# Performance work log

Measured on AMD Instinct MI355X. Metric: run time of the kernel, lower is better.

The kernel has to match this reference:

```python
import jax, jax.numpy as jnp
import numpy as np

B, C, H, W = 64, 64, 32, 32
K = 1024  # codebook_num
EPS = 1e-10


def setup_inputs() -> dict:
    key = jax.random.key(0)
    kz, kc = jax.random.split(key)
    z = jax.random.normal(kz, (B, C, H, W), dtype=jnp.float32)
    # nn.init.uniform_(codebook.weight, -1/K, 1/K)
    codebook = jax.random.uniform(kc, (K, C), dtype=jnp.float32, minval=-1.0 / K, maxval=1.0 / K)
    return {"z": z, "codebook": codebook}


def reference(z, codebook):
    Bz, Cz, Hz, Wz = z.shape
    flat_z = jnp.transpose(z, (0, 2, 3, 1)).reshape(-1, Cz)  # [N, C]
    dists = (jnp.sum(flat_z ** 2, axis=1, keepdims=True)
             + jnp.sum(codebook ** 2, axis=1)
             - 2.0 * flat_z @ codebook.T)
    indices = jnp.argmin(dists, axis=1)  # [N] int
    quantized_z = codebook[indices].reshape(Bz, Hz, Wz, Cz).transpose(0, 3, 1, 2)
    quantized_z_st = z + jax.lax.stop_gradient(quantized_z - z)
    # perplexity: probs = mean one-hot = histogram / N
    n = indices.shape[0]
    counts = jax.ops.segment_sum(jnp.ones((n,), dtype=jnp.float32), indices, num_segments=K)
    probs = counts / n
    perplexity = jnp.exp(-jnp.sum(probs * jnp.log(jnp.clip(probs, EPS))))
    return quantized_z, quantized_z_st, indices, perplexity
```

## Files before the change

### kernel.cpp

```cpp
#include <hip/hip_runtime.h>
#include <math.h>

#define NVEC   65536
#define CDIM   64
#define KBOOK  1024
#define NTOT   4194304


typedef __bf16 bf16x8 __attribute__((ext_vector_type(8)));
typedef float  f32x4  __attribute__((ext_vector_type(4)));

__global__ void prep_kernel(const float* __restrict__ cb, float* __restrict__ se,
                            int* __restrict__ hist, __bf16* __restrict__ cbT) {
    const int t = blockIdx.x * 256 + threadIdx.x;
    hist[t] = 0;
    const float* row = cb + t * CDIM;
    float r[8];
#pragma unroll
    for (int j = 0; j < 8; ++j) r[j] = __fmul_rn(row[j], row[j]);
#pragma unroll
    for (int i = 8; i < 64; i += 8)
#pragma unroll
        for (int j = 0; j < 8; ++j) r[j] = __fadd_rn(r[j], __fmul_rn(row[i + j], row[i + j]));
    se[t] = __fadd_rn(__fadd_rn(__fadd_rn(r[0], r[1]), __fadd_rn(r[2], r[3])),
                      __fadd_rn(__fadd_rn(r[4], r[5]), __fadd_rn(r[6], r[7])));
    const int tt = t >> 4, la = t & 15;
    __bf16* tb = cbT + (size_t)tt * 2048;
#pragma unroll
    for (int g = 0; g < 4; ++g)
#pragma unroll
        for (int j = 0; j < 8; ++j) {
            const float e0 = row[8 * g + j];
            const float e1 = row[32 + 8 * g + j];
            const __bf16 h0 = (__bf16)e0, h1 = (__bf16)e1;
            const int lo8 = (g * 16 + la) * 8 + j;
            tb[lo8]              = h0;
            tb[512 + lo8]        = h1;
            tb[1024 + lo8]       = (__bf16)(e0 - (float)h0);
            tb[1536 + lo8]       = (__bf16)(e1 - (float)h1);
        }
}

__launch_bounds__(256)
__attribute__((amdgpu_waves_per_eu(4, 4)))
__global__ void approx_kernel(const float* __restrict__ z, const __bf16* __restrict__ cbT,
                              const float* __restrict__ se,
                              unsigned int* __restrict__ cand) {
    const int tid = threadIdx.x;
    const int w = tid >> 6;
    const int l = tid & 63;
    const int la = l & 15;
    const int g  = l >> 4;
    const int n = blockIdx.x * 64 + w * 16 + la;
    const int b = n >> 10, hw = n & 1023;
    const float* zb = z + (size_t)b * (CDIM * 1024) + hw;

    bf16x8 mh0, ml0, mh1, ml1;
#pragma unroll
    for (int j = 0; j < 8; ++j) {
        {
            float zc = zb[(g * 8 + j) * 1024];
            float m  = -2.0f * zc;
            __bf16 h = (__bf16)m;
            mh0[j] = h; ml0[j] = (__bf16)(m - (float)h);
        }
        {
            float zc = zb[(32 + g * 8 + j) * 1024];
            float m  = -2.0f * zc;
            __bf16 h = (__bf16)m;
            mh1[j] = h; ml1[j] = (__bf16)(m - (float)h);
        }
    }

    float b1 = 3.4e38f, b2 = 3.4e38f;
    int   k1 = 0,       k2 = 0;
    const int kv = g * 4;
    const __bf16* tbase = cbT + (size_t)l * 8;

#define DECL_SLOT(s) bf16x8 ah0_##s, ah1_##s, al0_##s, al1_##s; f32x4 se_##s;
    DECL_SLOT(a) DECL_SLOT(b) DECL_SLOT(c) DECL_SLOT(d)
#undef DECL_SLOT

#define LOADT(s, ttv) { const int t_ = (ttv) & 63;                       \
        const __bf16* p_ = tbase + (size_t)t_ * 2048;                    \
        ah0_##s = *(const bf16x8*)(p_);                                  \
        ah1_##s = *(const bf16x8*)(p_ + 512);                            \
        al0_##s = *(const bf16x8*)(p_ + 1024);                           \
        al1_##s = *(const bf16x8*)(p_ + 1536);                           \
        se_##s  = *(const f32x4*)(se + t_ * 16 + kv); }

#define INS1(d_, kt_) { const bool c1 = (d_) < b1, c2 = (d_) < b2;       \
        b2 = c1 ? b1 : (c2 ? (d_) : b2);  k2 = c1 ? k1 : (c2 ? (kt_) : k2); \
        b1 = c1 ? (d_) : b1;              k1 = c1 ? (kt_) : k1; }

#define COMPT(s, ttv) { const int k0_ = (ttv) * 16;                      \
        f32x4 aA = se_##s; f32x4 aB = {0.f, 0.f, 0.f, 0.f};              \
        aA = __builtin_amdgcn_mfma_f32_16x16x32_bf16(ah0_##s, mh0, aA, 0, 0, 0); \
        aB = __builtin_amdgcn_mfma_f32_16x16x32_bf16(ah1_##s, mh1, aB, 0, 0, 0); \
        aA = __builtin_amdgcn_mfma_f32_16x16x32_bf16(al0_##s, mh0, aA, 0, 0, 0); \
        aB = __builtin_amdgcn_mfma_f32_16x16x32_bf16(al1_##s, mh1, aB, 0, 0, 0); \
        aA = __builtin_amdgcn_mfma_f32_16x16x32_bf16(ah0_##s, ml0, aA, 0, 0, 0); \
        aB = __builtin_amdgcn_mfma_f32_16x16x32_bf16(ah1_##s, ml1, aB, 0, 0, 0); \
        { const float d0_ = aA[0] + aB[0]; INS1(d0_, k0_ + kv)     }     \
        { const float d1_ = aA[1] + aB[1]; INS1(d1_, k0_ + kv + 1) }     \
        { const float d2_ = aA[2] + aB[2]; INS1(d2_, k0_ + kv + 2) }     \
        { const float d3_ = aA[3] + aB[3]; INS1(d3_, k0_ + kv + 3) } }

    LOADT(a, 0) LOADT(b, 1)
    for (int tt = 0; tt < 64; tt += 4) {
        LOADT(c, tt + 2) LOADT(d, tt + 3)
        COMPT(a, tt)     COMPT(b, tt + 1)
        LOADT(a, tt + 4) LOADT(b, tt + 5)
        COMPT(c, tt + 2) COMPT(d, tt + 3)
    }
#undef LOADT
#undef INS1
#undef COMPT

    cand[n * 4 + g] = (unsigned int)k1 | ((unsigned int)k2 << 16);
}

__global__ void rescore_kernel(const float* __restrict__ z, const float* __restrict__ cb,
                               const float* __restrict__ se,
                               const unsigned int* __restrict__ cand,
                               unsigned long long* __restrict__ keys,
                               int* __restrict__ hist, float* __restrict__ outIdxF) {
    __shared__ int lh[KBOOK];
    for (int i = threadIdx.x; i < KBOOK; i += 256) lh[i] = 0;
    __syncthreads();

    const int n = blockIdx.x * 256 + threadIdx.x;
    int ks[8];
#pragma unroll
    for (int g = 0; g < 4; ++g) {
        const unsigned int p = cand[n * 4 + g];
        ks[2 * g]     = (int)(p & 0xFFFFu);
        ks[2 * g + 1] = (int)(p >> 16);
    }
    const int b = n >> 10, hw = n & 1023;
    const float* zb = z + (size_t)b * (CDIM * 1024) + hw;

    float zx[64], r[8];
#pragma unroll
    for (int j = 0; j < 8; ++j) {
        const float zc = zb[j * 1024];
        zx[j] = zc + zc;
        r[j] = __fmul_rn(zc, zc);
    }
#pragma unroll
    for (int c = 8; c < 64; ++c) {
        const float zc = zb[c * 1024];
        zx[c] = zc + zc;
        r[c & 7] = __fadd_rn(r[c & 7], __fmul_rn(zc, zc));
    }
    const float sx = __fadd_rn(__fadd_rn(__fadd_rn(r[0], r[1]), __fadd_rn(r[2], r[3])),
                               __fadd_rn(__fadd_rn(r[4], r[5]), __fadd_rn(r[6], r[7])));

    float a[8];
#pragma unroll
    for (int i = 0; i < 8; ++i) a[i] = 0.0f;
    const float4* cb4 = (const float4*)cb;
#pragma unroll
    for (int q = 0; q < 16; ++q) {
#pragma unroll
        for (int i = 0; i < 8; ++i) {
            const float4 ev = cb4[ks[i] * 16 + q];
            a[i] = fmaf(zx[4 * q],     ev.x, a[i]);
            a[i] = fmaf(zx[4 * q + 1], ev.y, a[i]);
            a[i] = fmaf(zx[4 * q + 2], ev.z, a[i]);
            a[i] = fmaf(zx[4 * q + 3], ev.w, a[i]);
        }
    }
    unsigned long long best = ~0ull;
#pragma unroll
    for (int i = 0; i < 8; ++i) {
        const float d = __fsub_rn(__fadd_rn(sx, se[ks[i]]), a[i]);
        unsigned int ob = __float_as_uint(d);
        ob = (ob & 0x80000000u) ? ~ob : (ob | 0x80000000u);
        const unsigned long long key = ((unsigned long long)ob << 32) | (unsigned int)ks[i];
        if (key < best) best = key;
    }
    keys[n] = best;
    const int kbest = (int)(best & 0xFFFFFFFFu);
    outIdxF[n] = (float)kbest;
    atomicAdd(&lh[kbest], 1);
    __syncthreads();
    for (int i = threadIdx.x; i < KBOOK; i += 256)
        if (lh[i]) atomicAdd(&hist[i], lh[i]);
}

__global__ void scatter_kernel(const float* __restrict__ z, const float* __restrict__ cb,
                               const unsigned long long* __restrict__ keys,
                               const int* __restrict__ hist,
                               float* __restrict__ out) {
    const int o = (blockIdx.x * 256 + threadIdx.x) * 4;
    const int b = o >> 16, c = (o >> 10) & 63, hw = o & 1023;
    const int n = (b << 10) | hw;
    float q[4];
#pragma unroll
    for (int j = 0; j < 4; ++j) {
        const int k = (int)(keys[n + j] & 0xFFFFFFFFu);
        q[j] = cb[k * CDIM + c];
    }
    const float4 zv = *(const float4*)(z + o);
    *(float4*)(out + o) = make_float4(q[0], q[1], q[2], q[3]);
    float4 st;
    st.x = __fadd_rn(zv.x, __fsub_rn(q[0], zv.x));
    st.y = __fadd_rn(zv.y, __fsub_rn(q[1], zv.y));
    st.z = __fadd_rn(zv.z, __fsub_rn(q[2], zv.z));
    st.w = __fadd_rn(zv.w, __fsub_rn(q[3], zv.w));
    *(float4*)(out + NTOT + o) = st;

    if (blockIdx.x == 0) {
        __shared__ double partial[4];
        const int t = threadIdx.x;
        double term = 0.0;
#pragma unroll
        for (int j = 0; j < 4; ++j) {
            const int cnt = hist[t + 256 * j];
            if (cnt > 0) { const double p = (double)cnt / (double)NVEC; term += p * log(p); }
        }
        for (int off = 32; off > 0; off >>= 1) term += __shfl_down(term, off);
        if ((t & 63) == 0) partial[t >> 6] = term;
        __syncthreads();
        if (t == 0) {
            const double s = partial[0] + partial[1] + partial[2] + partial[3];
            out[2 * NTOT + NVEC] = (float)exp(-s);
        }
    }
}

extern "C" void kernel_launch(void* const* d_in, const int* in_sizes, int n_in,
                              void* d_out, int out_size, void* d_ws, size_t ws_size,
                              hipStream_t stream) {
    const float* z  = (const float*)d_in[0];
    const float* cb = (const float*)d_in[1];
    float* out = (float*)d_out;

    char* ws = (char*)d_ws;
    unsigned long long* keys = (unsigned long long*)(ws + 0);
    float* se   = (float*)(ws + 524288);
    int*   hist = (int*)(ws + 528384);

    char* outB = (char*)d_out;
    unsigned int* cand = (unsigned int*)(outB);
    __bf16* cbT = (__bf16*)(outB + (1 << 20));

    prep_kernel<<<4, 256, 0, stream>>>(cb, se, hist, cbT);
    approx_kernel<<<NVEC / 64, 256, 0, stream>>>(z, cbT, se, cand);
    rescore_kernel<<<NVEC / 256, 256, 0, stream>>>(z, cb, se, cand, keys, hist, out + 2 * NTOT);
    scatter_kernel<<<NTOT / 1024, 256, 0, stream>>>(z, cb, keys, hist, out);
}
```

Baseline: 173.6 us.

## Use scaled fp16 single-pass MFMA with error-bound filter and exact rescore fallback

The approximate distance pass drops the split-bf16 scheme, which needed six MFMAs per tile, in favour of one fp16 product with the codebook scaled by 16384 (two MFMAs per tile). Top-2 tracking packs each distance with its index into a single 32-bit key. An error-bound threshold, computed from ||x|| and the largest codebook norm, accepts the winner directly when the margin is large enough. Otherwise the vector goes onto a worklist, and a new kernel rescores it exactly in fp32 against all 1024 codes. This removes the 8-candidate rescore for every vector, but correctness now depends on the hand-derived bound and on fp16 range after scaling, and the worklist size depends on the data.

```diff
diff --git a/kernel.cpp b/kernel.cpp
--- a/kernel.cpp
+++ b/kernel.cpp
@@ -7,12 +7,16 @@
 #define NTOT   4194304
 
 
-typedef __bf16 bf16x8 __attribute__((ext_vector_type(8)));
-typedef float  f32x4  __attribute__((ext_vector_type(4)));
+typedef _Float16 f16x8 __attribute__((ext_vector_type(8)));
+typedef float    f32x4 __attribute__((ext_vector_type(4)));
 
 __global__ void prep_kernel(const float* __restrict__ cb, float* __restrict__ se,
-                            int* __restrict__ hist, __bf16* __restrict__ cbT) {
+                            int* __restrict__ hist, _Float16* __restrict__ cbT,
+                            float* __restrict__ se16, float* __restrict__ semax4,
+                            unsigned* __restrict__ wcount) {
+    __shared__ float lmax[4];
     const int t = blockIdx.x * 256 + threadIdx.x;
+    if (t == 0) *wcount = 0u;
     hist[t] = 0;
     const float* row = cb + t * CDIM;
     float r[8];
@@ -22,30 +26,38 @@
     for (int i = 8; i < 64; i += 8)
 #pragma unroll
         for (int j = 0; j < 8; ++j) r[j] = __fadd_rn(r[j], __fmul_rn(row[i + j], row[i + j]));
-    se[t] = __fadd_rn(__fadd_rn(__fadd_rn(r[0], r[1]), __fadd_rn(r[2], r[3])),
-                      __fadd_rn(__fadd_rn(r[4], r[5]), __fadd_rn(r[6], r[7])));
+    const float sev = __fadd_rn(__fadd_rn(__fadd_rn(r[0], r[1]), __fadd_rn(r[2], r[3])),
+                                __fadd_rn(__fadd_rn(r[4], r[5]), __fadd_rn(r[6], r[7])));
+    se[t] = sev;
+    se16[t] = sev * 16384.0f;
+    float m = sev;
+#pragma unroll
+    for (int off = 32; off > 0; off >>= 1) m = fmaxf(m, __shfl_xor(m, off));
+    if ((threadIdx.x & 63) == 0) lmax[threadIdx.x >> 6] = m;
+    __syncthreads();
+    if (threadIdx.x == 0)
+        semax4[blockIdx.x] = fmaxf(fmaxf(lmax[0], lmax[1]), fmaxf(lmax[2], lmax[3]));
     const int tt = t >> 4, la = t & 15;
-    __bf16* tb = cbT + (size_t)tt * 2048;
+    _Float16* tb = cbT + (size_t)tt * 1024;
 #pragma unroll
     for (int g = 0; g < 4; ++g)
 #pragma unroll
         for (int j = 0; j < 8; ++j) {
-            const float e0 = row[8 * g + j];
-            const float e1 = row[32 + 8 * g + j];
-            const __bf16 h0 = (__bf16)e0, h1 = (__bf16)e1;
+            const float e0 = row[8 * g + j] * 16384.0f;
+            const float e1 = row[32 + 8 * g + j] * 16384.0f;
             const int lo8 = (g * 16 + la) * 8 + j;
-            tb[lo8]              = h0;
-            tb[512 + lo8]        = h1;
-            tb[1024 + lo8]       = (__bf16)(e0 - (float)h0);
-            tb[1536 + lo8]       = (__bf16)(e1 - (float)h1);
+            tb[lo8]       = (_Float16)e0;
+            tb[512 + lo8] = (_Float16)e1;
         }
 }
 
 __launch_bounds__(256)
 __attribute__((amdgpu_waves_per_eu(4, 4)))
-__global__ void approx_kernel(const float* __restrict__ z, const __bf16* __restrict__ cbT,
-                              const float* __restrict__ se,
-                              unsigned int* __restrict__ cand) {
+__global__ void approx_kernel(const float* __restrict__ z, const _Float16* __restrict__ cbT,
+                              const float* __restrict__ se16, const float* __restrict__ semax4,
+                              unsigned* __restrict__ result, unsigned* __restrict__ wlist,
+                              unsigned* __restrict__ wcount, float* __restrict__ outIdxF,
+                              int* __restrict__ hist) {
     const int tid = threadIdx.x;
     const int w = tid >> 6;
     const int l = tid & 63;
@@ -55,56 +67,45 @@
     const int b = n >> 10, hw = n & 1023;
     const float* zb = z + (size_t)b * (CDIM * 1024) + hw;
 
-    bf16x8 mh0, ml0, mh1, ml1;
+    f16x8 mh0, mh1;
+    float psum = 0.0f;
 #pragma unroll
     for (int j = 0; j < 8; ++j) {
-        {
-            float zc = zb[(g * 8 + j) * 1024];
-            float m  = -2.0f * zc;
-            __bf16 h = (__bf16)m;
-            mh0[j] = h; ml0[j] = (__bf16)(m - (float)h);
-        }
-        {
-            float zc = zb[(32 + g * 8 + j) * 1024];
-            float m  = -2.0f * zc;
-            __bf16 h = (__bf16)m;
-            mh1[j] = h; ml1[j] = (__bf16)(m - (float)h);
-        }
-    }
-
-    float b1 = 3.4e38f, b2 = 3.4e38f;
-    int   k1 = 0,       k2 = 0;
+        {   float zc = zb[(g * 8 + j) * 1024];
+            mh0[j] = (_Float16)(-2.0f * zc);
+            psum = fmaf(zc, zc, psum); }
+        {   float zc = zb[(32 + g * 8 + j) * 1024];
+            mh1[j] = (_Float16)(-2.0f * zc);
+            psum = fmaf(zc, zc, psum); }
+    }
+
+    unsigned u1k = 0xFFFFFFFFu, u2k = 0xFFFFFFFFu;
     const int kv = g * 4;
-    const __bf16* tbase = cbT + (size_t)l * 8;
-
-#define DECL_SLOT(s) bf16x8 ah0_##s, ah1_##s, al0_##s, al1_##s; f32x4 se_##s;
+    const _Float16* tbase = cbT + (size_t)l * 8;
+
+#define DECL_SLOT(s) f16x8 ah0_##s, ah1_##s; f32x4 se_##s;
     DECL_SLOT(a) DECL_SLOT(b) DECL_SLOT(c) DECL_SLOT(d)
 #undef DECL_SLOT
 
 #define LOADT(s, ttv) { const int t_ = (ttv) & 63;                       \
-        const __bf16* p_ = tbase + (size_t)t_ * 2048;                    \
-        ah0_##s = *(const bf16x8*)(p_);                                  \
-        ah1_##s = *(const bf16x8*)(p_ + 512);                            \
-        al0_##s = *(const bf16x8*)(p_ + 1024);                           \
-        al1_##s = *(const bf16x8*)(p_ + 1536);                           \
-        se_##s  = *(const f32x4*)(se + t_ * 16 + kv); }
-
-#define INS1(d_, kt_) { const bool c1 = (d_) < b1, c2 = (d_) < b2;       \
-        b2 = c1 ? b1 : (c2 ? (d_) : b2);  k2 = c1 ? k1 : (c2 ? (kt_) : k2); \
-        b1 = c1 ? (d_) : b1;              k1 = c1 ? (kt_) : k1; }
+        const _Float16* p_ = tbase + (size_t)t_ * 1024;                  \
+        ah0_##s = *(const f16x8*)(p_);                                   \
+        ah1_##s = *(const f16x8*)(p_ + 512);                             \
+        se_##s  = *(const f32x4*)(se16 + t_ * 16 + kv); }
+
+#define PINS(acc_, r_, k0_) {                                            \
+        unsigned ub = __float_as_uint(acc_[r_]);                         \
+        ub = ((int)ub < 0) ? ~ub : (ub | 0x80000000u);                   \
+        const unsigned key = (ub & 0xFFFFFC00u) | (unsigned)((k0_) + kv + (r_)); \
+        const unsigned mx = (u1k > key) ? u1k : key;                     \
+        u1k = (u1k < key) ? u1k : key;                                   \
+        u2k = (u2k < mx) ? u2k : mx; }
 
 #define COMPT(s, ttv) { const int k0_ = (ttv) * 16;                      \
-        f32x4 aA = se_##s; f32x4 aB = {0.f, 0.f, 0.f, 0.f};              \
-        aA = __builtin_amdgcn_mfma_f32_16x16x32_bf16(ah0_##s, mh0, aA, 0, 0, 0); \
-        aB = __builtin_amdgcn_mfma_f32_16x16x32_bf16(ah1_##s, mh1, aB, 0, 0, 0); \
-        aA = __builtin_amdgcn_mfma_f32_16x16x32_bf16(al0_##s, mh0, aA, 0, 0, 0); \
-        aB = __builtin_amdgcn_mfma_f32_16x16x32_bf16(al1_##s, mh1, aB, 0, 0, 0); \
-        aA = __builtin_amdgcn_mfma_f32_16x16x32_bf16(ah0_##s, ml0, aA, 0, 0, 0); \
-        aB = __builtin_amdgcn_mfma_f32_16x16x32_bf16(ah1_##s, ml1, aB, 0, 0, 0); \
-        { const float d0_ = aA[0] + aB[0]; INS1(d0_, k0_ + kv)     }     \
-        { const float d1_ = aA[1] + aB[1]; INS1(d1_, k0_ + kv + 1) }     \
-        { const float d2_ = aA[2] + aB[2]; INS1(d2_, k0_ + kv + 2) }     \
-        { const float d3_ = aA[3] + aB[3]; INS1(d3_, k0_ + kv + 3) } }
+        f32x4 acc = se_##s;                                              \
+        acc = __builtin_amdgcn_mfma_f32_16x16x32_f16(ah0_##s, mh0, acc, 0, 0, 0); \
+        acc = __builtin_amdgcn_mfma_f32_16x16x32_f16(ah1_##s, mh1, acc, 0, 0, 0); \
+        PINS(acc, 0, k0_) PINS(acc, 1, k0_) PINS(acc, 2, k0_) PINS(acc, 3, k0_) }
 
     LOADT(a, 0) LOADT(b, 1)
     for (int tt = 0; tt < 64; tt += 4) {
@@ -114,38 +115,64 @@
         COMPT(c, tt + 2) COMPT(d, tt + 3)
     }
 #undef LOADT
-#undef INS1
+#undef PINS
 #undef COMPT
 
-    cand[n * 4 + g] = (unsigned int)k1 | ((unsigned int)k2 << 16);
-}
-
-__global__ void rescore_kernel(const float* __restrict__ z, const float* __restrict__ cb,
-                               const float* __restrict__ se,
-                               const unsigned int* __restrict__ cand,
-                               unsigned long long* __restrict__ keys,
-                               int* __restrict__ hist, float* __restrict__ outIdxF) {
-    __shared__ int lh[KBOOK];
-    for (int i = threadIdx.x; i < KBOOK; i += 256) lh[i] = 0;
-    __syncthreads();
-
-    const int n = blockIdx.x * 256 + threadIdx.x;
-    int ks[8];
-#pragma unroll
-    for (int g = 0; g < 4; ++g) {
-        const unsigned int p = cand[n * 4 + g];
-        ks[2 * g]     = (int)(p & 0xFFFFu);
-        ks[2 * g + 1] = (int)(p >> 16);
-    }
+#pragma unroll
+    for (int off = 16; off <= 32; off <<= 1) {
+        const unsigned p1 = __shfl_xor(u1k, off);
+        const unsigned p2 = __shfl_xor(u2k, off);
+        psum += __shfl_xor(psum, off);
+        const unsigned mx = (u1k > p1) ? u1k : p1;
+        u1k = (u1k < p1) ? u1k : p1;
+        const unsigned m2 = (u2k < p2) ? u2k : p2;
+        u2k = (m2 < mx) ? m2 : mx;
+    }
+
+    if (l < 16) {
+        const float sx = psum;
+        const float srt = sqrtf(fmaxf(fmaxf(semax4[0], semax4[1]),
+                                      fmaxf(semax4[2], semax4[3]))) * 1.0001f;
+        const float THR = 60.2f * sqrtf(sx) * srt + 1.97e-2f * sx + 0.165f;
+        const unsigned x1 = u1k & 0xFFFFFC00u, x2 = u2k & 0xFFFFFC00u;
+        const float f1 = __uint_as_float((x1 & 0x80000000u) ? (x1 & 0x7FFFFFFFu) : ~x1);
+        const float f2 = __uint_as_float((x2 & 0x80000000u) ? (x2 & 0x7FFFFFFFu) : ~x2);
+        const int k1 = (int)(u1k & 1023u);
+        if (f2 - f1 > THR) {
+            result[n] = (unsigned)k1;
+            outIdxF[n] = (float)k1;
+            atomicAdd(&hist[k1], 1);
+        } else {
+            const unsigned widx = atomicAdd(wcount, 1u);
+            wlist[widx] = (unsigned)n;
+        }
+    }
+}
+
+__launch_bounds__(256)
+__global__ void rescore2_kernel(const float* __restrict__ z, const float* __restrict__ cb,
+                                const float* __restrict__ se,
+                                const unsigned* __restrict__ wlist,
+                                const unsigned* __restrict__ wcount,
+                                unsigned* __restrict__ result, int* __restrict__ hist,
+                                float* __restrict__ outIdxF) {
+    const int cnt = (int)*wcount;
+    const int tid = threadIdx.x;
+    const int wv = tid >> 6, l = tid & 63;
+    const int base = (blockIdx.x * 4 + wv) * 4;
+    if (base >= cnt) return;
+    const int s = l >> 4, j = l & 15;
+    const int item = base + s;
+    const int n = (int)wlist[(item < cnt) ? item : base];
     const int b = n >> 10, hw = n & 1023;
     const float* zb = z + (size_t)b * (CDIM * 1024) + hw;
 
     float zx[64], r[8];
 #pragma unroll
-    for (int j = 0; j < 8; ++j) {
-        const float zc = zb[j * 1024];
-        zx[j] = zc + zc;
-        r[j] = __fmul_rn(zc, zc);
+    for (int jj = 0; jj < 8; ++jj) {
+        const float zc = zb[jj * 1024];
+        zx[jj] = zc + zc;
+        r[jj] = __fmul_rn(zc, zc);
     }
 #pragma unroll
     for (int c = 8; c < 64; ++c) {
@@ -156,41 +183,50 @@
     const float sx = __fadd_rn(__fadd_rn(__fadd_rn(r[0], r[1]), __fadd_rn(r[2], r[3])),
                                __fadd_rn(__fadd_rn(r[4], r[5]), __fadd_rn(r[6], r[7])));
 
-    float a[8];
-#pragma unroll
-    for (int i = 0; i < 8; ++i) a[i] = 0.0f;
+    unsigned long long best = ~0ull;
     const float4* cb4 = (const float4*)cb;
-#pragma unroll
-    for (int q = 0; q < 16; ++q) {
-#pragma unroll
-        for (int i = 0; i < 8; ++i) {
-            const float4 ev = cb4[ks[i] * 16 + q];
-            a[i] = fmaf(zx[4 * q],     ev.x, a[i]);
-            a[i] = fmaf(zx[4 * q + 1], ev.y, a[i]);
-            a[i] = fmaf(zx[4 * q + 2], ev.z, a[i]);
-            a[i] = fmaf(zx[4 * q + 3], ev.w, a[i]);
-        }
-    }
-    unsigned long long best = ~0ull;
-#pragma unroll
-    for (int i = 0; i < 8; ++i) {
-        const float d = __fsub_rn(__fadd_rn(sx, se[ks[i]]), a[i]);
-        unsigned int ob = __float_as_uint(d);
-        ob = (ob & 0x80000000u) ? ~ob : (ob | 0x80000000u);
-        const unsigned long long key = ((unsigned long long)ob << 32) | (unsigned int)ks[i];
-        if (key < best) best = key;
-    }
-    keys[n] = best;
-    const int kbest = (int)(best & 0xFFFFFFFFu);
-    outIdxF[n] = (float)kbest;
-    atomicAdd(&lh[kbest], 1);
-    __syncthreads();
-    for (int i = threadIdx.x; i < KBOOK; i += 256)
-        if (lh[i]) atomicAdd(&hist[i], lh[i]);
+    const int kb0 = j * 64;
+    for (int kk = 0; kk < 64; kk += 4) {
+        const int k = kb0 + kk;
+        float a0 = 0.f, a1 = 0.f, a2 = 0.f, a3 = 0.f;
+#pragma unroll
+        for (int q = 0; q < 16; ++q) {
+            const float4 e0 = cb4[(k + 0) * 16 + q];
+            const float4 e1 = cb4[(k + 1) * 16 + q];
+            const float4 e2 = cb4[(k + 2) * 16 + q];
+            const float4 e3 = cb4[(k + 3) * 16 + q];
+            a0 = fmaf(zx[4*q], e0.x, a0); a0 = fmaf(zx[4*q+1], e0.y, a0);
+            a0 = fmaf(zx[4*q+2], e0.z, a0); a0 = fmaf(zx[4*q+3], e0.w, a0);
+            a1 = fmaf(zx[4*q], e1.x, a1); a1 = fmaf(zx[4*q+1], e1.y, a1);
+            a1 = fmaf(zx[4*q+2], e1.z, a1); a1 = fmaf(zx[4*q+3], e1.w, a1);
+            a2 = fmaf(zx[4*q], e2.x, a2); a2 = fmaf(zx[4*q+1], e2.y, a2);
+            a2 = fmaf(zx[4*q+2], e2.z, a2); a2 = fmaf(zx[4*q+3], e2.w, a2);
+            a3 = fmaf(zx[4*q], e3.x, a3); a3 = fmaf(zx[4*q+1], e3.y, a3);
+            a3 = fmaf(zx[4*q+2], e3.z, a3); a3 = fmaf(zx[4*q+3], e3.w, a3);
+        }
+#define DKEY(ai, ki) { const float d_ = __fsub_rn(__fadd_rn(sx, se[ki]), ai);      \
+        unsigned ob = __float_as_uint(d_);                                         \
+        ob = (ob & 0x80000000u) ? ~ob : (ob | 0x80000000u);                        \
+        const unsigned long long key = ((unsigned long long)ob << 32) | (unsigned)(ki); \
+        if (key < best) best = key; }
+        DKEY(a0, k) DKEY(a1, k + 1) DKEY(a2, k + 2) DKEY(a3, k + 3)
+#undef DKEY
+    }
+#pragma unroll
+    for (int off = 1; off <= 8; off <<= 1) {
+        const unsigned long long o = __shfl_xor(best, off);
+        if (o < best) best = o;
+    }
+    if (j == 0 && item < cnt) {
+        const int kb = (int)(best & 0xFFFFFFFFull);
+        result[n] = (unsigned)kb;
+        outIdxF[n] = (float)kb;
+        atomicAdd(&hist[kb], 1);
+    }
 }
 
 __global__ void scatter_kernel(const float* __restrict__ z, const float* __restrict__ cb,
-                               const unsigned long long* __restrict__ keys,
+                               const unsigned* __restrict__ result,
                                const int* __restrict__ hist,
                                float* __restrict__ out) {
     const int o = (blockIdx.x * 256 + threadIdx.x) * 4;
@@ -199,7 +235,7 @@
     float q[4];
 #pragma unroll
     for (int j = 0; j < 4; ++j) {
-        const int k = (int)(keys[n + j] & 0xFFFFFFFFu);
+        const int k = (int)result[n + j];
         q[j] = cb[k * CDIM + c];
     }
     const float4 zv = *(const float4*)(z + o);
@@ -224,8 +260,8 @@
         if ((t & 63) == 0) partial[t >> 6] = term;
         __syncthreads();
         if (t == 0) {
-            const double s = partial[0] + partial[1] + partial[2] + partial[3];
-            out[2 * NTOT + NVEC] = (float)exp(-s);
+            const double sm = partial[0] + partial[1] + partial[2] + partial[3];
+            out[2 * NTOT + NVEC] = (float)exp(-sm);
         }
     }
 }
@@ -238,16 +274,23 @@
     float* out = (float*)d_out;
 
     char* ws = (char*)d_ws;
-    unsigned long long* keys = (unsigned long long*)(ws + 0);
+    unsigned* result = (unsigned*)ws;
     float* se   = (float*)(ws + 524288);
     int*   hist = (int*)(ws + 528384);
 
     char* outB = (char*)d_out;
-    unsigned int* cand = (unsigned int*)(outB);
-    __bf16* cbT = (__bf16*)(outB + (1 << 20));
-
-    prep_kernel<<<4, 256, 0, stream>>>(cb, se, hist, cbT);
-    approx_kernel<<<NVEC / 64, 256, 0, stream>>>(z, cbT, se, cand);
-    rescore_kernel<<<NVEC / 256, 256, 0, stream>>>(z, cb, se, cand, keys, hist, out + 2 * NTOT);
-    scatter_kernel<<<NTOT / 1024, 256, 0, stream>>>(z, cb, keys, hist, out);
-}
+    _Float16* cbT   = (_Float16*)(outB + (1 << 20));
+    unsigned* wcount = (unsigned*)(outB + 1572864);
+    float*    semax4 = (float*)(outB + 1572864 + 16);
+    float*    se16   = (float*)(outB + 1572864 + 4096);
+    unsigned* wlist  = (unsigned*)(outB + (2 << 20));
+
+    float* outIdxF = out + 2 * NTOT;
+
+    prep_kernel<<<4, 256, 0, stream>>>(cb, se, hist, cbT, se16, semax4, wcount);
+    approx_kernel<<<NVEC / 64, 256, 0, stream>>>(z, cbT, se16, semax4, result, wlist,
+                                                 wcount, outIdxF, hist);
+    rescore2_kernel<<<NVEC / 16, 256, 0, stream>>>(z, cb, se, wlist, wcount, result,
+                                                   hist, outIdxF);
+    scatter_kernel<<<NTOT / 1024, 256, 0, stream>>>(z, cb, result, hist, out);
+}
```

Result: slower. 406.9 us (+134.4%).
